# Performance work log

Hardware: AMD Instinct MI355X
Metric: run time of the kernel (lower is better)

## Reference

```python
import jax, jax.numpy as jnp
import numpy as np

N = 50000          # nodes
E_RAND = 590000    # random edges (+ N self-loops -> E = 640000)
IN_F = 128
OUT_F = 128
H, D = 8, 16       # num_heads, head_dim (H*D == OUT_F)
HOP = 5
ALPHA = 0.1
SLOPE = 0.2
EPS = 1e-5


def _layer_norm(x, g, b):
    mu = jnp.mean(x, axis=-1, keepdims=True)
    var = jnp.mean((x - mu) ** 2, axis=-1, keepdims=True)
    return (x - mu) * jax.lax.rsqrt(var + EPS) * g + b


def setup_inputs() -> dict:
    key = jax.random.key(0)
    ks = jax.random.split(key, 10)
    loops = jnp.arange(N, dtype=jnp.int32)  # self-loops -> no 0-in-degree nodes
    src = jnp.concatenate([loops, jax.random.randint(ks[0], (E_RAND,), 0, N, dtype=jnp.int32)])
    dst = jnp.concatenate([loops, jax.random.randint(ks[1], (E_RAND,), 0, N, dtype=jnp.int32)])
    s = 0.05  # xavier-like small init gain
    return {
        "feat": jax.random.normal(ks[2], (N, IN_F), jnp.float32),
        "src": src,
        "dst": dst,
        "w_head": jax.random.normal(ks[3], (OUT_F, IN_F), jnp.float32) * s,
        "w_tail": jax.random.normal(ks[4], (OUT_F, IN_F), jnp.float32) * s,
        "w_ent": jax.random.normal(ks[5], (OUT_F, IN_F), jnp.float32) * s,
        "attn": jax.random.normal(ks[6], (1, H, D), jnp.float32) * s,
        "ln1_g": jnp.ones((IN_F,), jnp.float32),
        "ln1_b": jnp.zeros((IN_F,), jnp.float32),
        "ln2_g": jnp.ones((OUT_F,), jnp.float32),
        "ln2_b": jnp.zeros((OUT_F,), jnp.float32),
        "ff_w1": jax.random.normal(ks[7], (4 * OUT_F, OUT_F), jnp.float32) * s,
        "ff_b1": jnp.zeros((4 * OUT_F,), jnp.float32),
        "ff_w2": jax.random.normal(ks[8], (OUT_F, 4 * OUT_F), jnp.float32) * s,
        "ff_b2": jnp.zeros((OUT_F,), jnp.float32),
    }


def _forward(src, dst, feat, w_head, w_tail, w_ent, attn,
             ln1_g, ln1_b, ln2_g, ln2_b, ff_w1, ff_b1, ff_w2, ff_b2):
    ones = jnp.ones(src.shape[0], jnp.float32)
    out_deg = jnp.clip(jax.ops.segment_sum(ones, src, num_segments=N), 1.0)  # [N]
    in_deg = jnp.clip(jax.ops.segment_sum(ones, dst, num_segments=N), 1.0)
    head_norm = out_deg ** -0.5
    tail_norm = in_deg ** 0.5
    log_in = jnp.log1p(in_deg)  # graph.dstdata['log_in'] (log of in-degree, set at graph build time)

    x = _layer_norm(feat, ln1_g, ln1_b)  # graph_layer_norm (feat_drop=0 in eval)
    fh = (x @ w_head.T).reshape(N, H, D) * head_norm[:, None, None]
    ft = (x @ w_tail.T).reshape(N, H, D) * head_norm[:, None, None]
    fe = (x @ w_ent.T).reshape(N, H, D) * head_norm[:, None, None]

    # edge attention logits: u_mul_v -> leaky_relu -> dot with attn vector
    lr = jax.nn.leaky_relu(fh[src] * ft[dst], SLOPE)  # [E,H,D]
    e = jnp.einsum('ehd,xhd->eh', lr, attn)           # [E,H]
    e = e * log_in[dst][:, None] / D                  # e_mul_v with log_in, / head_dim

    # edge softmax grouped by destination node, per head
    seg_max = jax.ops.segment_max(e, dst, num_segments=N)
    e_exp = jnp.exp(e - seg_max[dst])
    denom = jax.ops.segment_sum(e_exp, dst, num_segments=N)
    a = e_exp / denom[dst]                            # [E,H]

    # PPR diffusion (ppr_estimation), attn_drop=0 in eval
    feat0 = fe
    h = feat0
    for hop in range(HOP):
        if hop > 0:
            h = h * head_norm[:, None, None]
        m = h[src] * a[:, :, None]                    # [E,H,D] u_mul_e
        h = jax.ops.segment_sum(m, dst, num_segments=N)  # fn.sum
        h = h * tail_norm[:, None, None]
        h = (1.0 - ALPHA) * h + ALPHA * feat0

    rst = h + feat.reshape(N, H, D)  # res_fc is Identity since in_feats == out_feats
    rst = rst.reshape(N, OUT_F)
    ff = _layer_norm(rst, ln2_g, ln2_b)
    ff = jax.nn.relu(ff @ ff_w1.T + ff_b1) @ ff_w2.T + ff_b2  # PositionWiseFeedForward
    return ff + rst


def reference(feat, src, dst, w_head, w_tail, w_ent, attn, ln1_g, ln1_b,
              ln2_g, ln2_b, ff_w1, ff_b1, ff_w2, ff_b2):
    return _forward(src, dst, feat, w_head, w_tail, w_ent, attn,
                    ln1_g, ln1_b, ln2_g, ln2_b, ff_w1, ff_b1, ff_w2, ff_b2)
```

## Files before the change

kernel.cpp:

```cpp
#include <hip/hip_runtime.h>
#include <hip/hip_bf16.h>
#include <hip/hip_fp16.h>

typedef __attribute__((ext_vector_type(8))) short bf16x8;
typedef __attribute__((ext_vector_type(4))) float f32x4;
typedef unsigned int uint32;

#define F 128
#define HOPS 5
#define LDS_STRIDE 68
#define W1_STRIDE 136
#define W2_STRIDE 72
#define TB_STRIDE 72

__device__ __forceinline__ float b2f(__hip_bfloat16 h) { return __bfloat162float(h); }
__device__ __forceinline__ __hip_bfloat16 f2b(float f) { return __float2bfloat16(f); }

__device__ __forceinline__ float load_in(const void* p, size_t i, int isbf) {
    return isbf ? __bfloat162float(((const __hip_bfloat16*)p)[i]) : ((const float*)p)[i];
}

__device__ __forceinline__ float bflo(uint32 u) { union { uint32 i; float f; } v; v.i = u << 16; return v.f; }
__device__ __forceinline__ float bfhi(uint32 u) { union { uint32 i; float f; } v; v.i = u & 0xffff0000u; return v.f; }
__device__ __forceinline__ uint32 packbf2(float a, float b) {
    __hip_bfloat16 ha = f2b(a), hb = f2b(b);
    unsigned short ua = *(unsigned short*)&ha, ub = *(unsigned short*)&hb;
    return ((uint32)ub << 16) | ua;
}

__device__ __forceinline__ int xcd_id() {
    unsigned v;
    asm volatile("s_getreg_b32 %0, hwreg(HW_REG_XCC_ID)" : "=s"(v));
    return (int)(v & 7);
}

__device__ __forceinline__ float edge_dot2(uint4 gv, const float* c1, const float* c2) {
    float acc = 0.f, acc2 = 0.f;
    uint32 us[4] = {gv.x, gv.y, gv.z, gv.w};
    #pragma unroll
    for (int k = 0; k < 4; ++k) {
        float f0 = bflo(us[k]), f1 = bfhi(us[k]);
        acc  = fmaf(c1[2 * k],     f0,        acc);
        acc2 = fmaf(c2[2 * k],     fabsf(f0), acc2);
        acc  = fmaf(c1[2 * k + 1], f1,        acc);
        acc2 = fmaf(c2[2 * k + 1], fabsf(f1), acc2);
    }
    return acc + acc2;
}

__global__ void detect_k(const uint32* __restrict__ w, int* flag) {
    __shared__ int cnt[256];
    int t = threadIdx.x;
    uint32 x = w[t * 97];
    int e_low = (x >> 7) & 0xFF;
    cnt[t] = (e_low >= 110 && e_low <= 135) ? 1 : 0;
    __syncthreads();
    for (int s = 128; s > 0; s >>= 1) {
        if (t < s) cnt[t] += cnt[t + s];
        __syncthreads();
    }
    if (t == 0) flag[0] = (cnt[0] >= 160) ? 1 : 0;
}

__global__ void fused_pre_k(const int* __restrict__ src, const int* __restrict__ dst,
                            int* in8, int* out1, uint32* __restrict__ pack, int E,
                            const void* __restrict__ feat, const void* __restrict__ ln1g,
                            const void* __restrict__ ln1b,
                            const void* __restrict__ w_head, const void* __restrict__ w_tail,
                            const void* __restrict__ w_ent, const void* __restrict__ ff_w1,
                            const void* __restrict__ ff_w2, const void* __restrict__ attn,
                            const void* __restrict__ ff_b1, const void* __restrict__ ff_b2,
                            const int* __restrict__ flag,
                            __hip_bfloat16* __restrict__ wblob, float* __restrict__ fblob,
                            __hip_bfloat16* __restrict__ x_bf,
                            int nbDeg, int nbLn, int N) {
    int bid = blockIdx.x;
    if (bid < nbDeg) {
        int base = bid * 2048 + threadIdx.x;
        int slice = xcd_id();
        int idx[8], d[8], s[8], r[8];
#pragma unroll
        for (int k = 0; k < 8; ++k) idx[k] = base + k * 256;
#pragma unroll
        for (int k = 0; k < 8; ++k)
            if (idx[k] < E) { d[k] = dst[idx[k]]; s[k] = src[idx[k]]; }
#pragma unroll
        for (int k = 0; k < 8; ++k)
            if (idx[k] < E) r[k] = atomicAdd(&in8[slice * N + d[k]], 1);
#pragma unroll
        for (int k = 0; k < 8; ++k)
            if (idx[k] < E) atomicAdd(&out1[s[k]], 1);
#pragma unroll
        for (int k = 0; k < 8; ++k)
            if (idx[k] < E) pack[idx[k]] = (uint32)r[k] | ((uint32)slice << 24);
        return;
    }
    if (bid < nbDeg + nbLn) {
        int w = (bid - nbDeg) * 4 + (threadIdx.x >> 6);
        if (w >= N) return;
        int isbf = flag[0];
        int t = threadIdx.x & 63;
        float v0 = load_in(feat, (size_t)w * F + t, isbf);
        float v1 = load_in(feat, (size_t)w * F + t + 64, isbf);
        float s = v0 + v1, sq = v0 * v0 + v1 * v1;
        for (int m = 1; m < 64; m <<= 1) { s += __shfl_xor(s, m, 64); sq += __shfl_xor(sq, m, 64); }
        float mu = s * (1.0f / F);
        float var = fmaxf(sq * (1.0f / F) - mu * mu, 0.0f);
        float r = rsqrtf(var + 1e-5f);
        x_bf[(size_t)w * F + t]      = f2b((v0 - mu) * r * load_in(ln1g, t, isbf) + load_in(ln1b, t, isbf));
        x_bf[(size_t)w * F + t + 64] = f2b((v1 - mu) * r * load_in(ln1g, t + 64, isbf) + load_in(ln1b, t + 64, isbf));
        return;
    }
    {
        int i = (bid - nbDeg - nbLn) * 256 + threadIdx.x;
        int isbf = flag[0];
        if (i < 180224) {
            const void* srcp; int j;
            if (i < 16384)       { srcp = w_head; j = i; }
            else if (i < 32768)  { srcp = w_tail; j = i - 16384; }
            else if (i < 49152)  { srcp = w_ent;  j = i - 32768; }
            else if (i < 114688) { srcp = ff_w1;  j = i - 49152; }
            else                 { srcp = ff_w2;  j = i - 114688; }
            wblob[i] = f2b(load_in(srcp, j, isbf));
        } else if (i < 180992) {
            int k = i - 180224;
            const void* srcp; int j;
            if (k < 128)      { srcp = attn;  j = k; }
            else if (k < 640) { srcp = ff_b1; j = k - 128; }
            else              { srcp = ff_b2; j = k - 640; }
            fblob[k] = load_in(srcp, j, isbf);
        }
    }
}

__global__ void scan1_k(const int* __restrict__ in8, int* partial, int* blk_sum, int N) {
    __shared__ int sh[256];
    int t = threadIdx.x;
    int i = blockIdx.x * 256 + t;
    int c = 0;
    if (i < N) {
#pragma unroll
        for (int s = 0; s < 8; ++s) c += in8[s * N + i];
    }
    sh[t] = c;
    __syncthreads();
    for (int o = 1; o < 256; o <<= 1) {
        int v = (t >= o) ? sh[t - o] : 0;
        __syncthreads();
        sh[t] += v;
        __syncthreads();
    }
    if (i < N) partial[i] = sh[t] - c;
    if (t == 255) blk_sum[blockIdx.x] = sh[255];
}

__global__ void scan2_k(const int* __restrict__ blk_sum, int* blk_off, int nb,
                        int* row_ptr, int N) {
    __shared__ int sh[256];
    int t = threadIdx.x;
    if (nb <= 256) {
        int v = (t < nb) ? blk_sum[t] : 0;
        sh[t] = v;
        __syncthreads();
        for (int o = 1; o < 256; o <<= 1) {
            int u = (t >= o) ? sh[t - o] : 0;
            __syncthreads();
            sh[t] += u;
            __syncthreads();
        }
        if (t < nb) blk_off[t] = sh[t] - v;
        if (t == 255) row_ptr[N] = sh[255];
    } else if (t == 0) {
        int run = 0;
        for (int b = 0; b < nb; ++b) { blk_off[b] = run; run += blk_sum[b]; }
        row_ptr[N] = run;
    }
}

__global__ void scan3_norms_k(const int* __restrict__ partial, const int* __restrict__ blk_off,
                              const int* __restrict__ in8, const int* __restrict__ out1,
                              int* row_ptr, int* soff, float* head_norm, float* tail_norm,
                              float* log_in, int N) {
    int i = blockIdx.x * 256 + threadIdx.x;
    if (i >= N) return;
    row_ptr[i] = partial[i] + blk_off[blockIdx.x];
    int run = 0;
#pragma unroll
    for (int s = 0; s < 8; ++s) { soff[s * N + i] = run; run += in8[s * N + i]; }
    int od = out1[i];
    float id = fmaxf((float)run, 1.0f);
    float odf = fmaxf((float)od, 1.0f);
    head_norm[i] = rsqrtf(odf);
    tail_norm[i] = sqrtf(id);
    log_in[i] = log1pf(id);
}

__global__ void scan3f_k(const int* __restrict__ partial, const int* __restrict__ blk_sum,
                         int nb, const int* __restrict__ in8, const int* __restrict__ out1,
                         int* row_ptr, int* soff, float* head_norm, float* tail_norm,
                         float* log_in, int N) {
    __shared__ int bs[256];
    int t = threadIdx.x;
    bs[t] = (t < nb) ? blk_sum[t] : 0;
    __syncthreads();
    for (int o = 1; o < 256; o <<= 1) {
        int v = (t >= o) ? bs[t - o] : 0;
        __syncthreads();
        bs[t] += v;
        __syncthreads();
    }
    if (blockIdx.x == 0 && t == 0) row_ptr[N] = bs[nb - 1];
    int boff = (blockIdx.x == 0) ? 0 : bs[blockIdx.x - 1];
    int i = blockIdx.x * 256 + t;
    if (i >= N) return;
    row_ptr[i] = partial[i] + boff;
    int run = 0;
#pragma unroll
    for (int s = 0; s < 8; ++s) { soff[s * N + i] = run; run += in8[s * N + i]; }
    int od = out1[i];
    float id = fmaxf((float)run, 1.0f);
    float odf = fmaxf((float)od, 1.0f);
    head_norm[i] = rsqrtf(odf);
    tail_norm[i] = sqrtf(id);
    log_in[i] = log1pf(id);
}

__global__ void fused_mid_k(const int* __restrict__ src, const int* __restrict__ dst,
                            const int* __restrict__ row_ptr, const int* __restrict__ soff,
                            const uint32* __restrict__ pack, int* __restrict__ csr_src,
                            int E, int N, int nbSc, int Mb,
                            const __hip_bfloat16* __restrict__ X,
                            const __hip_bfloat16* __restrict__ Wall,
                            const float* __restrict__ head_norm,
                            __hip_bfloat16* __restrict__ fh,
                            __hip_bfloat16* __restrict__ ft,
                            uint32* __restrict__ fe_bf) {
    __shared__ __align__(16) char smem[2 * 64 * W1_STRIDE * 2];
    int bid = blockIdx.x;
    if (bid < nbSc) {
        int base = bid * 2048 + threadIdx.x;
#pragma unroll
        for (int k = 0; k < 8; ++k) {
            int i = base + k * 256;
            if (i < E) {
                int d = dst[i];
                uint32 pk = pack[i];
                int s = (int)(pk >> 24);
                int r = (int)(pk & 0xFFFFFFu);
                csr_src[row_ptr[d] + soff[s * N + d] + r] = src[i];
            }
        }
        return;
    }
    int pb = bid - nbSc;
    int g = pb / Mb;
    int bm = (pb - g * Mb) * 64;
    __hip_bfloat16* lx = (__hip_bfloat16*)smem;
    __hip_bfloat16* lw = (__hip_bfloat16*)(smem + 64 * W1_STRIDE * 2);
    float* eps = (float*)smem;
    int tid = threadIdx.x;
    int wv = tid >> 6, lane = tid & 63;
    int lr = lane & 15, quad = lane >> 4;
    int wsel = g >> 1;
    int wcb = (g & 1) * 64;
    {
        const __hip_bfloat16* xs = X + (size_t)bm * F;
        size_t maxe = (size_t)N * F;
#pragma unroll
        for (int i = 0; i < 4; ++i) {
            int idx = i * 2048 + tid * 8;
            int n = idx >> 7, k = idx & 127;
            size_t gi = (size_t)bm * F + idx;
            uint4 v = (gi + 8 <= maxe) ? *(const uint4*)(xs + idx)
                                       : *(const uint4*)(X + maxe - 8);
            *(uint4*)&lx[n * W1_STRIDE + k] = v;
        }
        const __hip_bfloat16* ws = Wall + ((size_t)wsel * F + wcb) * F;
#pragma unroll
        for (int i = 0; i < 4; ++i) {
            int idx = i * 2048 + tid * 8;
            int n = idx >> 7, k = idx & 127;
            *(uint4*)&lw[n * W1_STRIDE + k] = *(const uint4*)(ws + idx);
        }
    }
    __syncthreads();
    f32x4 acc[4] = {{0,0,0,0},{0,0,0,0},{0,0,0,0},{0,0,0,0}};
#pragma unroll
    for (int ks = 0; ks < 4; ++ks) {
        bf16x8 a = *reinterpret_cast<const bf16x8*>(&lx[(wv * 16 + lr) * W1_STRIDE + ks * 32 + quad * 8]);
#pragma unroll
        for (int j = 0; j < 4; ++j) {
            bf16x8 bb = *reinterpret_cast<const bf16x8*>(&lw[(j * 16 + lr) * W1_STRIDE + ks * 32 + quad * 8]);
            acc[j] = __builtin_amdgcn_mfma_f32_16x16x32_bf16(a, bb, acc[j], 0, 0, 0);
        }
    }
    __syncthreads();
    int rl = wv * 16 + quad * 4;
#pragma unroll
    for (int j = 0; j < 4; ++j)
#pragma unroll
        for (int r = 0; r < 4; ++r)
            eps[(rl + r) * LDS_STRIDE + j * 16 + lr] = acc[j][r];
    __syncthreads();
    int tr = tid >> 4, tc = (tid & 15) * 4;
#pragma unroll
    for (int p = 0; p < 4; ++p) {
        int row_l = p * 16 + tr;
        int grow = bm + row_l;
        if (grow >= N) continue;
        float4 v = *(const float4*)&eps[row_l * LDS_STRIDE + tc];
        float hn = head_norm[grow];
        v.x *= hn; v.y *= hn; v.z *= hn; v.w *= hn;
        size_t idx = (size_t)grow * F + wcb + tc;
        uint2 u; u.x = packbf2(v.x, v.y); u.y = packbf2(v.z, v.w);
        __hip_bfloat16* dstp = (wsel == 0) ? fh : (wsel == 1) ? ft : (__hip_bfloat16*)fe_bf;
        *(uint2*)&dstp[idx] = u;
    }
}

__global__ void attn_hop0_k(const int* __restrict__ csr_src, const int* __restrict__ row_ptr,
                            const uint32* __restrict__ fh2, const uint32* __restrict__ ft2,
                            const float* __restrict__ attn_f, const float* __restrict__ log_in,
                            const float* __restrict__ tail_norm, const float* __restrict__ head_norm,
                            const uint32* __restrict__ fe_bf,
                            __half* __restrict__ e_h, float* __restrict__ inv_arr,
                            uint32* __restrict__ out_bf, int N) {
    int w = blockIdx.x * (blockDim.x >> 6) + (threadIdx.x >> 6);
    if (w >= N) return;
    int t = threadIdx.x & 63;
    int g = t >> 4, j = t & 15;
    int b = row_ptr[w], e = row_ptr[w + 1];
    uint4 fr = ((const uint4*)ft2)[(size_t)w * 16 + j];
    float ftf[8] = {bflo(fr.x), bfhi(fr.x), bflo(fr.y), bfhi(fr.y),
                    bflo(fr.z), bfhi(fr.z), bflo(fr.w), bfhi(fr.w)};
    float c1[8], c2[8];
#pragma unroll
    for (int k = 0; k < 8; ++k) {
        float at = attn_f[8 * j + k];
        c1[k] = 0.6f * at * ftf[k];
        c2[k] = 0.4f * at * fabsf(ftf[k]);
    }
    float scale = log_in[w] * (1.0f / 16.0f);
    float m = -1e30f;
    for (int p0 = b; p0 < e; p0 += 8) {
        int pa = p0 + g, pb = p0 + 4 + g;
        bool oka = pa < e, okb = pb < e;
        int sa = csr_src[oka ? pa : b];
        int sb = csr_src[okb ? pb : b];
        uint4 ga = ((const uint4*)fh2)[(size_t)sa * 16 + j];
        uint4 gb = ((const uint4*)fh2)[(size_t)sb * 16 + j];
        float ra = edge_dot2(ga, c1, c2);
        float rb = edge_dot2(gb, c1, c2);
        ra += __shfl_xor(ra, 1, 64);
        rb += __shfl_xor(rb, 1, 64);
        float la = ra * scale, lb = rb * scale;
        if (oka) { if (!(j & 1)) e_h[(size_t)pa * 8 + (j >> 1)] = __float2half(la); m = fmaxf(m, la); }
        if (okb) { if (!(j & 1)) e_h[(size_t)pb * 8 + (j >> 1)] = __float2half(lb); m = fmaxf(m, lb); }
    }
    m = fmaxf(m, __shfl_xor(m, 16, 64));
    m = fmaxf(m, __shfl_xor(m, 32, 64));
    int h = t >> 3;
    int il = t & 7;
    float mh = __shfl(m, h * 2, 64);
    float sum = 0.f, a0 = 0.f, a1 = 0.f;
    for (int p = b; p < e; p += 8) {
        int qo = p + il;
        bool okm = qo < e;
        int qm = okm ? qo : b;
        float lg = __half2float(e_h[(size_t)qm * 8 + h]);
        float exm = okm ? __expf(lg - mh) : 0.f;
        if (okm) e_h[(size_t)qm * 8 + h] = __float2half(exm);
        int srcs[8];
#pragma unroll
        for (int i = 0; i < 8; ++i) {
            int qi = p + i;
            srcs[i] = csr_src[qi < e ? qi : b];
        }
        uint32 rows[8];
#pragma unroll
        for (int i = 0; i < 8; ++i) rows[i] = fe_bf[(size_t)srcs[i] * 64 + t];
#pragma unroll
        for (int i = 0; i < 8; ++i) {
            float exi = __shfl(exm, (t & 56) | i, 64);
            sum += exi;
            a0 = fmaf(bflo(rows[i]), exi, a0);
            a1 = fmaf(bfhi(rows[i]), exi, a1);
        }
    }
    float inv = 1.0f / fmaxf(sum, 1e-30f);
    if ((t & 7) == 0) inv_arr[(size_t)w * 8 + h] = inv;
    float tl = tail_norm[w] * 0.9f * inv;
    uint32 fe_l = fe_bf[(size_t)w * 64 + t];
    float r0 = tl * a0 + 0.1f * bflo(fe_l);
    float r1 = tl * a1 + 0.1f * bfhi(fe_l);
    float hn = head_norm[w];
    out_bf[(size_t)w * 64 + t] = packbf2(r0 * hn, r1 * hn);
}

__global__ void hop_k(const uint32* __restrict__ gsrc2, const __half* __restrict__ e_h,
                      const float* __restrict__ inv_arr,
                      const int* __restrict__ csr_src, const int* __restrict__ row_ptr,
                      const float* __restrict__ tail_norm, const float* __restrict__ head_norm,
                      const uint32* __restrict__ fe_bf, const void* __restrict__ feat,
                      const void* __restrict__ ln2g, const void* __restrict__ ln2b,
                      const int* __restrict__ flag,
                      uint32* __restrict__ out_bf, float* __restrict__ out_f32,
                      int last, int N) {
    int w = blockIdx.x * 8 + (threadIdx.x >> 5);
    if (w >= N) return;
    int l = threadIdx.x & 31;
    int h = l >> 2;
    int b = row_ptr[w], e = row_ptr[w + 1];
    float inv = inv_arr[(size_t)w * 8 + h];
    float a0 = 0.f, a1 = 0.f, a2 = 0.f, a3 = 0.f;
    int p = b;
    for (; p + 8 <= e; p += 8) {
        int s[8]; float av[8]; uint2 gg[8];
#pragma unroll
        for (int i = 0; i < 8; ++i) s[i] = csr_src[p + i];
#pragma unroll
        for (int i = 0; i < 8; ++i) av[i] = __half2float(e_h[(size_t)(p + i) * 8 + h]);
#pragma unroll
        for (int i = 0; i < 8; ++i) gg[i] = ((const uint2*)gsrc2)[(size_t)s[i] * 32 + l];
#pragma unroll
        for (int i = 0; i < 8; ++i) {
            a0 += bflo(gg[i].x) * av[i]; a1 += bfhi(gg[i].x) * av[i];
            a2 += bflo(gg[i].y) * av[i]; a3 += bfhi(gg[i].y) * av[i];
        }
    }
    if (p < e) {
        int s[8]; float av[8]; uint2 gg[8];
#pragma unroll
        for (int i = 0; i < 8; ++i) {
            int q = p + i;
            bool ok = q < e;
            int q2 = ok ? q : b;
            s[i] = csr_src[q2];
            av[i] = ok ? __half2float(e_h[(size_t)q * 8 + h]) : 0.f;
        }
#pragma unroll
        for (int i = 0; i < 8; ++i) gg[i] = ((const uint2*)gsrc2)[(size_t)s[i] * 32 + l];
#pragma unroll
        for (int i = 0; i < 8; ++i) {
            a0 += bflo(gg[i].x) * av[i]; a1 += bfhi(gg[i].x) * av[i];
            a2 += bflo(gg[i].y) * av[i]; a3 += bfhi(gg[i].y) * av[i];
        }
    }
    float tl = tail_norm[w] * 0.9f * inv;
    uint2 feu = ((const uint2*)fe_bf)[(size_t)w * 32 + l];
    float r0 = tl * a0 + 0.1f * bflo(feu.x);
    float r1 = tl * a1 + 0.1f * bfhi(feu.x);
    float r2 = tl * a2 + 0.1f * bflo(feu.y);
    float r3 = tl * a3 + 0.1f * bfhi(feu.y);
    if (last) {
        int isbf = flag[0];
        float4 o;
        if (isbf) {
            uint2 fu = ((const uint2*)feat)[(size_t)w * 32 + l];
            o.x = r0 + bflo(fu.x); o.y = r1 + bfhi(fu.x);
            o.z = r2 + bflo(fu.y); o.w = r3 + bfhi(fu.y);
        } else {
            float4 fv = ((const float4*)feat)[(size_t)w * 32 + l];
            o.x = r0 + fv.x; o.y = r1 + fv.y; o.z = r2 + fv.z; o.w = r3 + fv.w;
        }
        ((float4*)out_f32)[(size_t)w * 32 + l] = o;
        float s2 = o.x + o.y + o.z + o.w;
        float sq = o.x * o.x + o.y * o.y + o.z * o.z + o.w * o.w;
#pragma unroll
        for (int mm = 1; mm < 32; mm <<= 1) {
            s2 += __shfl_xor(s2, mm, 64);
            sq += __shfl_xor(sq, mm, 64);
        }
        float mu = s2 * (1.0f / F);
        float var = fmaxf(sq * (1.0f / F) - mu * mu, 0.0f);
        float rr = rsqrtf(var + 1e-5f);
        float g0 = load_in(ln2g, 4 * l + 0, isbf), g1 = load_in(ln2g, 4 * l + 1, isbf);
        float g2 = load_in(ln2g, 4 * l + 2, isbf), g3 = load_in(ln2g, 4 * l + 3, isbf);
        float b0 = load_in(ln2b, 4 * l + 0, isbf), b1 = load_in(ln2b, 4 * l + 1, isbf);
        float b2 = load_in(ln2b, 4 * l + 2, isbf), b3 = load_in(ln2b, 4 * l + 3, isbf);
        uint2 u;
        u.x = packbf2((o.x - mu) * rr * g0 + b0, (o.y - mu) * rr * g1 + b1);
        u.y = packbf2((o.z - mu) * rr * g2 + b2, (o.w - mu) * rr * g3 + b3);
        ((uint2*)out_bf)[(size_t)w * 32 + l] = u;
    } else {
        float hn = head_norm[w];
        uint2 u;
        u.x = packbf2(r0 * hn, r1 * hn);
        u.y = packbf2(r2 * hn, r3 * hn);
        ((uint2*)out_bf)[(size_t)w * 32 + l] = u;
    }
}

__global__ __launch_bounds__(256, 2)
void ffn_fused_k(const __hip_bfloat16* __restrict__ Y, const __hip_bfloat16* __restrict__ W1,
                 const __hip_bfloat16* __restrict__ W2, const float* __restrict__ b1f,
                 const float* __restrict__ b2f, const float* __restrict__ rst,
                 const int* __restrict__ flag, void* __restrict__ out, int N) {
    __shared__ __align__(16) char smem[45056];
    __hip_bfloat16* lw1 = (__hip_bfloat16*)smem;
    __hip_bfloat16* lw2 = (__hip_bfloat16*)(smem + 17408);
    __hip_bfloat16* tb  = (__hip_bfloat16*)(smem + 35840);
    float* eps = (float*)smem;
    int tid = threadIdx.x;
    int wv = tid >> 6, lane = tid & 63;
    int lr = lane & 15, quad = lane >> 4;
    int bm = blockIdx.x * 64;
    int row_a = bm + wv * 16 + lr;
    if (row_a >= N) row_a = N - 1;
    bf16x8 ay[4];
    {
        const __hip_bfloat16* yr = Y + (size_t)row_a * F + quad * 8;
#pragma unroll
        for (int ks = 0; ks < 4; ++ks) ay[ks] = *reinterpret_cast<const bf16x8*>(yr + ks * 32);
    }
    f32x4 o[8];
#pragma unroll
    for (int j = 0; j < 8; ++j) o[j] = (f32x4){0,0,0,0};
    __hip_bfloat16* tbuf = tb + wv * (16 * TB_STRIDE);
    for (int c = 0; c < 8; ++c) {
        int nb0 = c * 64;
        __syncthreads();
        {
            const __hip_bfloat16* s1 = W1 + (size_t)nb0 * F;
#pragma unroll
            for (int i = 0; i < 4; ++i) {
                int idx = i * 2048 + tid * 8;
                int n = idx >> 7, k = idx & 127;
                *(uint4*)&lw1[n * W1_STRIDE + k] = *(const uint4*)(s1 + idx);
            }
#pragma unroll
            for (int i = 0; i < 4; ++i) {
                int idx = i * 2048 + tid * 8;
                int r = idx >> 6, k2 = idx & 63;
                *(uint4*)&lw2[r * W2_STRIDE + k2] = *(const uint4*)(W2 + (size_t)r * 512 + nb0 + k2);
            }
        }
        __syncthreads();
        f32x4 t[4] = {{0,0,0,0},{0,0,0,0},{0,0,0,0},{0,0,0,0}};
#pragma unroll
        for (int ks = 0; ks < 4; ++ks) {
#pragma unroll
            for (int j = 0; j < 4; ++j) {
                bf16x8 bb = *reinterpret_cast<const bf16x8*>(&lw1[(j * 16 + lr) * W1_STRIDE + ks * 32 + quad * 8]);
                t[j] = __builtin_amdgcn_mfma_f32_16x16x32_bf16(ay[ks], bb, t[j], 0, 0, 0);
            }
        }
#pragma unroll
        for (int j = 0; j < 4; ++j) {
            float bias = b1f[nb0 + 16 * j + lr];
#pragma unroll
            for (int r = 0; r < 4; ++r) {
                float v = fmaxf(t[j][r] + bias, 0.f);
                tbuf[(quad * 4 + r) * TB_STRIDE + j * 16 + lr] = f2b(v);
            }
        }
#pragma unroll
        for (int ks2 = 0; ks2 < 2; ++ks2) {
            bf16x8 at = *reinterpret_cast<const bf16x8*>(&tbuf[lr * TB_STRIDE + ks2 * 32 + quad * 8]);
#pragma unroll
            for (int j2 = 0; j2 < 8; ++j2) {
                bf16x8 bb = *reinterpret_cast<const bf16x8*>(&lw2[(j2 * 16 + lr) * W2_STRIDE + ks2 * 32 + quad * 8]);
                o[j2] = __builtin_amdgcn_mfma_f32_16x16x32_bf16(at, bb, o[j2], 0, 0, 0);
            }
        }
    }
    __syncthreads();
    int rl = wv * 16 + quad * 4;
#pragma unroll
    for (int j = 0; j < 8; ++j)
#pragma unroll
        for (int r = 0; r < 4; ++r)
            eps[(rl + r) * 132 + j * 16 + lr] = o[j][r];
    __syncthreads();
    int isbf = flag[0];
#pragma unroll
    for (int p = 0; p < 8; ++p) {
        int idx = p * 1024 + tid * 4;
        int row_l = idx >> 7, col = idx & 127;
        int grow = bm + row_l;
        if (grow >= N) continue;
        float4 v = *(const float4*)&eps[row_l * 132 + col];
        float4 bias = *(const float4*)&b2f[col];
        float4 rv = *(const float4*)&rst[(size_t)grow * F + col];
        v.x += bias.x + rv.x; v.y += bias.y + rv.y;
        v.z += bias.z + rv.z; v.w += bias.w + rv.w;
        size_t gidx = (size_t)grow * F + col;
        if (isbf) {
            uint2 u; u.x = packbf2(v.x, v.y); u.y = packbf2(v.z, v.w);
            *(uint2*)&((__hip_bfloat16*)out)[gidx] = u;
        } else {
            *(float4*)&((float*)out)[gidx] = v;
        }
    }
}

extern "C" void kernel_launch(void* const* d_in, const int* in_sizes, int n_in,
                              void* d_out, int out_size, void* d_ws, size_t ws_size,
                              hipStream_t stream) {
    if (n_in < 15) return;
    const void* feat = d_in[0];
    const int* src = (const int*)d_in[1];
    const int* dst = (const int*)d_in[2];
    const void* w_head = d_in[3];
    const void* w_tail = d_in[4];
    const void* w_ent  = d_in[5];
    const void* attn   = d_in[6];
    const void* ln1_g  = d_in[7];
    const void* ln1_b  = d_in[8];
    const void* ln2_g  = d_in[9];
    const void* ln2_b  = d_in[10];
    const void* ff_w1  = d_in[11];
    const void* ff_b1  = d_in[12];
    const void* ff_w2  = d_in[13];
    const void* ff_b2  = d_in[14];

    const int N = in_sizes[0] / F;
    const int E = in_sizes[1];
    (void)out_size;

    char* base = (char*)d_ws;
    size_t off = 0;
    auto alloc = [&](size_t bytes) -> void* {
        void* r = base + off;
        off += (bytes + 255) & ~(size_t)255;
        return r;
    };
    int* zr        = (int*)alloc((size_t)9 * N * 4);
    int* in8 = zr, * out1 = zr + 8 * N;
    int* soff      = (int*)alloc((size_t)8 * N * 4);
    int* row_ptr   = (int*)alloc((size_t)(N + 1) * 4);
    int* partial   = (int*)alloc((size_t)N * 4);
    int* blk_sum   = (int*)alloc((size_t)1024 * 4);
    int* blk_off   = (int*)alloc((size_t)1024 * 4);
    int* flag      = (int*)alloc(256);
    float* head_norm = (float*)alloc((size_t)N * 4);
    float* tail_norm = (float*)alloc((size_t)N * 4);
    float* log_in    = (float*)alloc((size_t)N * 4);
    float* inv_arr   = (float*)alloc((size_t)N * 8 * 4);
    int* csr_src   = (int*)alloc((size_t)E * 4);
    uint32* pack   = (uint32*)alloc((size_t)E * 4);
    __hip_bfloat16* wh_bf = (__hip_bfloat16*)alloc((size_t)F * F * 2);
    __hip_bfloat16* wt_bf = (__hip_bfloat16*)alloc((size_t)F * F * 2);
    __hip_bfloat16* we_bf = (__hip_bfloat16*)alloc((size_t)F * F * 2);
    __hip_bfloat16* w1_bf = (__hip_bfloat16*)alloc((size_t)512 * F * 2);
    __hip_bfloat16* w2_bf = (__hip_bfloat16*)alloc((size_t)F * 512 * 2);
    float* attn_f    = (float*)alloc((size_t)F * 4);
    float* b1f       = (float*)alloc((size_t)512 * 4);
    float* b2f_      = (float*)alloc((size_t)F * 4);
    __hip_bfloat16* x_bf = (__hip_bfloat16*)alloc((size_t)N * F * 2);
    __hip_bfloat16* fh   = (__hip_bfloat16*)alloc((size_t)N * F * 2);
    __hip_bfloat16* ftb  = (__hip_bfloat16*)alloc((size_t)N * F * 2);
    uint32* fe_bf = (uint32*)alloc((size_t)N * F * 2);
    uint32* hA_bf = (uint32*)alloc((size_t)N * F * 2);
    uint32* hB_bf = (uint32*)alloc((size_t)N * F * 2);
    float* rst = (float*)alloc((size_t)N * F * 4);
    __hip_bfloat16* y_bf = (__hip_bfloat16*)hA_bf;
    __half* e_h = (__half*)x_bf;
    (void)wt_bf; (void)we_bf;
    if (off > ws_size) return;

    const int Mb = (N + 63) / 64;
    const int nodeBlocks = (N + 3) / 4;
    const int hopBlocks = (N + 7) / 8;
    const int nb = (N + 255) / 256;
    const int nbDeg = (E + 2047) / 2048;
    const int nbLn  = (N + 3) / 4;
    const int nbCvt = (180992 + 255) / 256;

    detect_k<<<1, 256, 0, stream>>>((const uint32*)feat, flag);
    hipMemsetAsync(zr, 0, (size_t)9 * N * 4, stream);

    fused_pre_k<<<nbDeg + nbLn + nbCvt, 256, 0, stream>>>(
        src, dst, in8, out1, pack, E,
        feat, ln1_g, ln1_b,
        w_head, w_tail, w_ent, ff_w1, ff_w2, attn, ff_b1, ff_b2,
        flag, wh_bf, attn_f, x_bf, nbDeg, nbLn, N);

    scan1_k<<<nb, 256, 0, stream>>>(in8, partial, blk_sum, N);
    if (nb <= 256) {
        scan3f_k<<<nb, 256, 0, stream>>>(partial, blk_sum, nb, in8, out1,
                                         row_ptr, soff, head_norm, tail_norm, log_in, N);
    } else {
        scan2_k<<<1, 256, 0, stream>>>(blk_sum, blk_off, nb, row_ptr, N);
        scan3_norms_k<<<nb, 256, 0, stream>>>(partial, blk_off, in8, out1,
                                              row_ptr, soff, head_norm, tail_norm, log_in, N);
    }

    const int nbSc = (E + 2047) / 2048;
    fused_mid_k<<<nbSc + Mb * 6, 256, 0, stream>>>(
        src, dst, row_ptr, soff, pack, csr_src, E, N, nbSc, Mb,
        x_bf, wh_bf, head_norm, fh, ftb, fe_bf);

    attn_hop0_k<<<nodeBlocks, 256, 0, stream>>>(csr_src, row_ptr, (const uint32*)fh,
                                                (const uint32*)ftb, attn_f, log_in,
                                                tail_norm, head_norm, fe_bf,
                                                e_h, inv_arr, hA_bf, N);

    const uint32* gsrc = hA_bf;
    uint32* bufs[2] = {hA_bf, hB_bf};
    for (int hop = 1; hop < HOPS; ++hop) {
        int last = (hop == HOPS - 1);
        uint32* dst_bf = last ? (uint32*)y_bf : bufs[hop & 1];
        hop_k<<<hopBlocks, 256, 0, stream>>>(gsrc, e_h, inv_arr, csr_src, row_ptr, tail_norm,
                                             head_norm, fe_bf, feat, ln2_g, ln2_b, flag,
                                             dst_bf, rst, last, N);
        if (!last) gsrc = dst_bf;
    }

    ffn_fused_k<<<Mb, 256, 0, stream>>>(y_bf, w1_bf, w2_bf, b1f, b2f_, rst, flag, d_out, N);
}
```

Measured before the change: 419.6 us.

## Fuse hop-0 softmax passes by dropping segment max and clamping exponent

Computes exp of the attention logits directly in the first edge loop, with the exponent clamped at 30, instead of first finding the per-head max. The same loop also accumulates the weighted neighbour features, which removes the second pass over the edges. That pass re-read and rewrote the fp16 edge logits and reloaded the source indices. The trade-off is reliance on logits staying bounded; unnormalized fp16 exponentials could overflow for large logits.

```diff
diff --git a/kernel.cpp b/kernel.cpp
--- a/kernel.cpp
+++ b/kernel.cpp
@@ -329,6 +329,7 @@
     if (w >= N) return;
     int t = threadIdx.x & 63;
     int g = t >> 4, j = t & 15;
+    int h = t >> 3;
     int b = row_ptr[w], e = row_ptr[w + 1];
     uint4 fr = ((const uint4*)ft2)[(size_t)w * 16 + j];
     float ftf[8] = {bflo(fr.x), bfhi(fr.x), bflo(fr.y), bfhi(fr.y),
@@ -341,7 +342,7 @@
         c2[k] = 0.4f * at * fabsf(ftf[k]);
     }
     float scale = log_in[w] * (1.0f / 16.0f);
-    float m = -1e30f;
+    float sum = 0.f, a0 = 0.f, a1 = 0.f;
     for (int p0 = b; p0 < e; p0 += 8) {
         int pa = p0 + g, pb = p0 + 4 + g;
         bool oka = pa < e, okb = pb < e;
@@ -353,38 +354,19 @@
         float rb = edge_dot2(gb, c1, c2);
         ra += __shfl_xor(ra, 1, 64);
         rb += __shfl_xor(rb, 1, 64);
-        float la = ra * scale, lb = rb * scale;
-        if (oka) { if (!(j & 1)) e_h[(size_t)pa * 8 + (j >> 1)] = __float2half(la); m = fmaxf(m, la); }
-        if (okb) { if (!(j & 1)) e_h[(size_t)pb * 8 + (j >> 1)] = __float2half(lb); m = fmaxf(m, lb); }
-    }
-    m = fmaxf(m, __shfl_xor(m, 16, 64));
-    m = fmaxf(m, __shfl_xor(m, 32, 64));
-    int h = t >> 3;
-    int il = t & 7;
-    float mh = __shfl(m, h * 2, 64);
-    float sum = 0.f, a0 = 0.f, a1 = 0.f;
-    for (int p = b; p < e; p += 8) {
-        int qo = p + il;
-        bool okm = qo < e;
-        int qm = okm ? qo : b;
-        float lg = __half2float(e_h[(size_t)qm * 8 + h]);
-        float exm = okm ? __expf(lg - mh) : 0.f;
-        if (okm) e_h[(size_t)qm * 8 + h] = __float2half(exm);
-        int srcs[8];
+        float exa = oka ? __expf(fminf(ra * scale, 30.f)) : 0.f;
+        float exb = okb ? __expf(fminf(rb * scale, 30.f)) : 0.f;
+        if (oka && !(j & 1)) e_h[(size_t)pa * 8 + (j >> 1)] = __float2half(exa);
+        if (okb && !(j & 1)) e_h[(size_t)pb * 8 + (j >> 1)] = __float2half(exb);
 #pragma unroll
         for (int i = 0; i < 8; ++i) {
-            int qi = p + i;
-            srcs[i] = csr_src[qi < e ? qi : b];
-        }
-        uint32 rows[8];
-#pragma unroll
-        for (int i = 0; i < 8; ++i) rows[i] = fe_bf[(size_t)srcs[i] * 64 + t];
-#pragma unroll
-        for (int i = 0; i < 8; ++i) {
-            float exi = __shfl(exm, (t & 56) | i, 64);
+            int qi = p0 + i;
+            int qs = csr_src[qi < e ? qi : b];
+            uint32 row = fe_bf[(size_t)qs * 64 + t];
+            float exi = __shfl(i < 4 ? exa : exb, (i & 3) * 16 + 2 * h, 64);
             sum += exi;
-            a0 = fmaf(bflo(rows[i]), exi, a0);
-            a1 = fmaf(bfhi(rows[i]), exi, a1);
+            a0 = fmaf(bflo(row), exi, a0);
+            a1 = fmaf(bfhi(row), exi, a1);
         }
     }
     float inv = 1.0f / fmaxf(sum, 1e-30f);
```

Measured after the change: 423.5 us. About the same (+0.9%).
